# Optimization experiments

Hardware: AMD Instinct MI355X
Metric: run time of the kernel (lower is better)

The kernel has to match this reference:

```python
import jax, jax.numpy as jnp
import numpy as np

N = 50000       # nodes
E = 800000      # edges (before self-loops)
G = 512         # graphs in batch
IN_DIM = 128
OUT_DIM = 8
DIMS = [(IN_DIM, 32), (32, 64), (64, 128), (128, 64)]
EPS = 1e-5


def setup_inputs() -> dict:
    key = jax.random.key(0)
    ks = jax.random.split(key, 40)
    def nrm(k, shape, s=0.05):
        return jax.random.normal(k, shape, jnp.float32) * s
    inp = {}
    inp["x"] = jax.random.normal(ks[0], (N, IN_DIM), jnp.float32)
    inp["edge_index"] = jax.random.randint(ks[1], (2, E), 0, N, dtype=jnp.int32)
    inp["batch"] = jnp.sort(jax.random.randint(ks[2], (N,), 0, G, dtype=jnp.int32))
    for i, (din, dout) in enumerate(DIMS, 1):
        inp[f"W{i}"]  = nrm(ks[3 * i + 0], (din, dout))
        inp[f"as{i}"] = nrm(ks[3 * i + 1], (dout,))
        inp[f"ad{i}"] = nrm(ks[3 * i + 2], (dout,))
        inp[f"b{i}"]  = jnp.zeros((dout,), jnp.float32)
        inp[f"g{i}"]  = jnp.ones((dout,), jnp.float32)   # BN gamma
        inp[f"be{i}"] = jnp.zeros((dout,), jnp.float32)  # BN beta
    inp["Wf"] = nrm(ks[20], (64, 32)); inp["bf"] = jnp.zeros((32,), jnp.float32)
    inp["Wc"] = nrm(ks[21], (32, OUT_DIM)); inp["bc"] = jnp.zeros((OUT_DIM,), jnp.float32)
    return inp


def gat_conv(x, src, dst, W, a_s, a_d, b):
    """PyG GATConv, heads=1: linear (no bias) -> per-edge attention with
    leaky_relu(0.2) -> segment softmax over incoming edges -> scatter-add -> bias."""
    h = x @ W                                   # [N, F]
    a_src = h @ a_s                             # [N]
    a_dst = h @ a_d                             # [N]
    e = jax.nn.leaky_relu(a_src[src] + a_dst[dst], 0.2)   # [E+N]
    m = jax.ops.segment_max(e, dst, num_segments=N)
    w = jnp.exp(e - m[dst])
    denom = jax.ops.segment_sum(w, dst, num_segments=N)
    alpha = w / denom[dst]                      # self-loops guarantee denom > 0
    out = jax.ops.segment_sum(alpha[:, None] * h[src], dst, num_segments=N)
    return out + b


def batch_norm(x, g, be):
    mu = x.mean(axis=0)
    var = x.var(axis=0)                         # biased, as torch training BN
    return (x - mu) * jax.lax.rsqrt(var + EPS) * g + be


def reference(x, edge_index, batch,
              W1, as1, ad1, b1, g1, be1,
              W2, as2, ad2, b2, g2, be2,
              W3, as3, ad3, b3, g3, be3,
              W4, as4, ad4, b4, g4, be4,
              Wf, bf, Wc, bc):
    loops = jnp.arange(N, dtype=edge_index.dtype)
    src = jnp.concatenate([edge_index[0], loops])   # GATConv adds self-loops
    dst = jnp.concatenate([edge_index[1], loops])
    params = [(W1, as1, ad1, b1, g1, be1), (W2, as2, ad2, b2, g2, be2),
              (W3, as3, ad3, b3, g3, be3), (W4, as4, ad4, b4, g4, be4)]
    h = x
    for (W, a_s, a_d, b, g, be) in params:
        h = jax.nn.leaky_relu(gat_conv(h, src, dst, W, a_s, a_d, b), 0.01)
        h = batch_norm(h, g, be)
    pooled = jax.ops.segment_sum(h, batch, num_segments=G)   # global_add_pool
    z = jax.nn.leaky_relu(pooled @ Wf + bf, 0.01)
    return jax.nn.sigmoid(z @ Wc + bc)
```

## Files before the change

kernel.cpp:

```cpp
#include <hip/hip_runtime.h>
#include <math.h>

constexpr int BLK = 256;
constexpr int NBLKA = 256;
constexpr int NSH = 16;

static inline int cdiv(long a, long b) { return (int)((a + b - 1) / b); }

typedef __attribute__((ext_vector_type(8))) short short8;
typedef __attribute__((ext_vector_type(4))) float floatx4;

__device__ __forceinline__ unsigned short f2bf(float f) {
    unsigned u = __float_as_uint(f);
    unsigned r = u + 0x7fffu + ((u >> 16) & 1u);
    return (unsigned short)(r >> 16);
}
__device__ __forceinline__ float bf2f(unsigned short s) {
    return __uint_as_float(((unsigned)s) << 16);
}


__global__ void histA_k(const int* __restrict__ dst, int* __restrict__ histg,
                        int E, int nbkt, int chunk) {
    __shared__ int h[256];
    int tid = threadIdx.x, z = blockIdx.x;
    h[tid] = 0;
    __syncthreads();
    int e0 = z * chunk, e1 = min(E, e0 + chunk);
    for (int e = e0 + tid; e < e1; e += BLK) atomicAdd(&h[dst[e] >> 8], 1);
    __syncthreads();
    if (tid < nbkt) histg[z * nbkt + tid] = h[tid];
}

__global__ void blk_scan2_k(int* __restrict__ histg, int* __restrict__ bsum, int nbkt) {
    __shared__ int s[BLK];
    int t = threadIdx.x, b = blockIdx.x;
    int v = histg[t * nbkt + b];
    s[t] = v;
    __syncthreads();
    for (int o = 1; o < BLK; o <<= 1) {
        int tv = (t >= o) ? s[t - o] : 0;
        __syncthreads();
        s[t] += tv;
        __syncthreads();
    }
    histg[t * nbkt + b] = s[t] - v;
    if (t == BLK - 1) bsum[b] = s[t];
}

__global__ void scan_base_k(const int* __restrict__ bsum, int* __restrict__ bucket_base,
                            int nbkt, int E, int* __restrict__ gs, int* __restrict__ ge,
                            int G, float* __restrict__ bnstats) {
    __shared__ int s[BLK];
    int t = threadIdx.x;
    int v = (t < nbkt) ? bsum[t] : 0;
    s[t] = v;
    __syncthreads();
    for (int o = 1; o < BLK; o <<= 1) {
        int tv = (t >= o) ? s[t - o] : 0;
        __syncthreads();
        s[t] += tv;
        __syncthreads();
    }
    if (t < nbkt) bucket_base[t] = s[t] - v;
    if (t == 0) bucket_base[nbkt] = E;
    for (int i = t; i < G; i += BLK) { gs[i] = 0x7fffffff; ge[i] = -1; }
    for (int i = t; i < 4 * NSH * 256; i += BLK) bnstats[i] = 0.f;
}

__global__ void csrB_k(const unsigned* __restrict__ ebkt, const int* __restrict__ bucket_base,
                       int* __restrict__ off, unsigned short* __restrict__ csr,
                       const int* __restrict__ batch, int* __restrict__ gs,
                       int* __restrict__ ge, int N, int E, int nbkt) {
    __shared__ int dg[256];
    __shared__ int sc[256];
    int t = threadIdx.x, b = blockIdx.x;
    int n0 = b << 8;
    int cnt = min(256, N - n0);
    dg[t] = (t < cnt) ? 1 : 0;
    __syncthreads();
    int e0 = bucket_base[b], e1 = bucket_base[b + 1];
    for (int e = e0 + t; e < e1; e += BLK) atomicAdd(&dg[ebkt[e] >> 16], 1);
    __syncthreads();
    int d = dg[t];
    sc[t] = d;
    __syncthreads();
    for (int o = 1; o < BLK; o <<= 1) {
        int tv = (t >= o) ? sc[t - o] : 0;
        __syncthreads();
        sc[t] += tv;
        __syncthreads();
    }
    int loff = sc[t] - d;
    int csrbase = e0 + n0;
    if (t < cnt) {
        off[n0 + t] = csrbase + loff;
        csr[csrbase + loff] = (unsigned short)(n0 + t);
        dg[t] = loff + 1;
    }
    if (b == nbkt - 1 && t == 0) off[N] = E + N;
    int n = n0 + t;
    if (n < N) {
        int bb = batch[n];
        if (n == 0) gs[bb] = 0;
        else {
            int pb = batch[n - 1];
            if (pb != bb) { gs[bb] = n; ge[pb] = n - 1; }
        }
        if (n == N - 1) ge[bb] = N - 1;
    }
    __syncthreads();
    for (int e = e0 + t; e < e1; e += BLK) {
        unsigned w = ebkt[e];
        int pos = atomicAdd(&dg[w >> 16], 1);
        csr[csrbase + pos] = (unsigned short)(w & 0xffff);
    }
}

template <int K, int NOUT, bool AFP32, bool HASBN, bool DOTS, bool FIN>
__device__ __forceinline__ void gemm_body(int bx, const void* __restrict__ av,
                           const float* __restrict__ W,
                           const float* __restrict__ a_s, const float* __restrict__ a_d,
                           const float* __restrict__ bnst, const float* __restrict__ g_prev,
                           const float* __restrict__ be_prev, float invN,
                           const float* __restrict__ bias_l,
                           unsigned short* __restrict__ hb,
                           float* __restrict__ asrc, float* __restrict__ adst,
                           float* __restrict__ bn_out, int N) {
    constexpr int KF = K / 32;
    constexpr int NY = NOUT / 16;
    __shared__ float s_sca[K], s_scc[K];
    __shared__ float s_rs[DOTS ? K : 1], s_rd[DOTS ? K : 1], s_bd[2];
    __shared__ float sst[FIN ? 2 * NOUT : 1];
    int tid = threadIdx.x;
    if (FIN && tid < 2 * NOUT) sst[tid] = 0.f;
    if (tid < K) {
        float a = 1.f, c = 0.f;
        if (HASBN) {
            float su = 0.f, sq = 0.f;
#pragma unroll
            for (int s = 0; s < NSH; ++s) {
                su += bnst[s * 256 + tid];
                sq += bnst[s * 256 + 128 + tid];
            }
            float mu = su * invN;
            float var = sq * invN - mu * mu;
            a = g_prev[tid] * rsqrtf(var + 1e-5f);
            c = be_prev[tid] - mu * a;
        }
        s_sca[tid] = a; s_scc[tid] = c;
        if (DOTS) {
            const float* wr = W + (long)tid * NOUT;
            float rs = 0.f, rd = 0.f;
            for (int f = 0; f < NOUT; ++f) {
                float w = wr[f];
                rs += w * a_s[f];
                rd += w * a_d[f];
            }
            s_rs[tid] = rs; s_rd[tid] = rd;
        }
    }
    __syncthreads();
    if constexpr (DOTS) {
        if (tid < 2) {
            const float* r = tid ? s_rd : s_rs;
            float b = 0.f;
            for (int k = 0; k < K; ++k) b += s_scc[k] * r[k];
            s_bd[tid] = b;
        }
        __syncthreads();
    }

    int wave = tid >> 6;
    int lane = tid & 63;
    int quad = lane >> 4;
    int r16 = lane & 15;
    int blockbase = bx * 128;

    short8 afr[2][KF];
    bool valid[2];
#pragma unroll
    for (int rt = 0; rt < 2; ++rt) {
        int tilebase = blockbase + wave * 32 + rt * 16;
        valid[rt] = tilebase < N;
        if (!valid[rt]) continue;
        int arow = min(tilebase + r16, N - 1);
        if (AFP32) {
            const float* xr = (const float*)av + (long)arow * K;
#pragma unroll
            for (int kk = 0; kk < KF; ++kk) {
                float4 x0 = *(const float4*)(xr + kk * 32 + quad * 8);
                float4 x1 = *(const float4*)(xr + kk * 32 + quad * 8 + 4);
                short8 a;
                a[0] = (short)f2bf(x0.x); a[1] = (short)f2bf(x0.y);
                a[2] = (short)f2bf(x0.z); a[3] = (short)f2bf(x0.w);
                a[4] = (short)f2bf(x1.x); a[5] = (short)f2bf(x1.y);
                a[6] = (short)f2bf(x1.z); a[7] = (short)f2bf(x1.w);
                afr[rt][kk] = a;
            }
        } else {
            const unsigned short* hr = (const unsigned short*)av + (long)arow * K;
#pragma unroll
            for (int kk = 0; kk < KF; ++kk)
                afr[rt][kk] = *(const short8*)(hr + kk * 32 + quad * 8);
        }
        if constexpr (DOTS) {
            float ds = 0.f, dd = 0.f;
#pragma unroll
            for (int kk = 0; kk < KF; ++kk) {
                int kb = kk * 32 + quad * 8;
#pragma unroll
                for (int j = 0; j < 8; ++j) {
                    int k = kb + j;
                    float a = bf2f((unsigned short)afr[rt][kk][j]) * s_sca[k];
                    ds += a * s_rs[k];
                    dd += a * s_rd[k];
                }
            }
            ds += __shfl_xor(ds, 16, 64); ds += __shfl_xor(ds, 32, 64);
            dd += __shfl_xor(dd, 16, 64); dd += __shfl_xor(dd, 32, 64);
            int drow = tilebase + r16;
            if (quad == 0 && drow < N) {
                asrc[drow] = ds + s_bd[0];
                adst[drow] = dd + s_bd[1];
            }
        }
    }

#pragma unroll
    for (int y = 0; y < NY; ++y) {
        int col = y * 16 + r16;
        short8 bfr[KF];
        float biasp = 0.f;
#pragma unroll
        for (int kk = 0; kk < KF; ++kk) {
            short8 b;
#pragma unroll
            for (int j = 0; j < 8; ++j) {
                int k = kk * 32 + quad * 8 + j;
                float w = W[(long)k * NOUT + col];
                b[j] = (short)f2bf(s_sca[k] * w);
                biasp += s_scc[k] * w;
            }
            bfr[kk] = b;
        }
        biasp += __shfl_xor(biasp, 16, 64);
        biasp += __shfl_xor(biasp, 32, 64);
        if (FIN) biasp += bias_l[col];

        float sS = 0.f, sQ = 0.f;
#pragma unroll
        for (int rt = 0; rt < 2; ++rt) {
            if (!valid[rt]) continue;
            int tilebase = blockbase + wave * 32 + rt * 16;
            floatx4 acc = {0.f, 0.f, 0.f, 0.f};
#pragma unroll
            for (int kk = 0; kk < KF; ++kk)
                acc = __builtin_amdgcn_mfma_f32_16x16x32_bf16(afr[rt][kk], bfr[kk], acc, 0, 0, 0);
#pragma unroll
            for (int rr = 0; rr < 4; ++rr) {
                int srow = tilebase + quad * 4 + rr;
                if (srow < N) {
                    float v = acc[rr] + biasp;
                    if (FIN) {
                        v = v > 0.f ? v : 0.01f * v;
                        sS += v; sQ += v * v;
                    }
                    hb[(long)srow * NOUT + col] = f2bf(v);
                }
            }
        }
        if constexpr (FIN) {
            sS += __shfl_xor(sS, 16, 64); sS += __shfl_xor(sS, 32, 64);
            sQ += __shfl_xor(sQ, 16, 64); sQ += __shfl_xor(sQ, 32, 64);
            if (quad == 0) {
                atomicAdd(&sst[col], sS);
                atomicAdd(&sst[NOUT + col], sQ);
            }
        }
    }
    if constexpr (FIN) {
        __syncthreads();
        if (tid < 2 * NOUT) {
            float* base = bn_out + (bx & (NSH - 1)) * 256;
            int idx = (tid < NOUT) ? tid : (128 + tid - NOUT);
            atomicAdd(&base[idx], sst[tid]);
        }
    }
}

template <int K, int NOUT, bool AFP32, bool HASBN, bool DOTS, bool FIN>
__launch_bounds__(256)
__global__ void gemm_fused(const void* __restrict__ av, const float* __restrict__ W,
                           const float* __restrict__ a_s, const float* __restrict__ a_d,
                           const float* __restrict__ bnst, const float* __restrict__ g_prev,
                           const float* __restrict__ be_prev, float invN,
                           const float* __restrict__ bias_l,
                           unsigned short* __restrict__ hb,
                           float* __restrict__ asrc, float* __restrict__ adst,
                           float* __restrict__ bn_out, int N) {
    gemm_body<K, NOUT, AFP32, HASBN, DOTS, FIN>(blockIdx.x, av, W, a_s, a_d, bnst, g_prev,
                                                be_prev, invN, bias_l, hb, asrc, adst,
                                                bn_out, N);
}

__launch_bounds__(256)
__global__ void scatter_gemm0_k(const int* __restrict__ src, const int* __restrict__ dst,
                                const int* __restrict__ histg, const int* __restrict__ bucket_base,
                                unsigned* __restrict__ ebkt, int E, int nbkt, int chunk,
                                const float* __restrict__ x, const float* __restrict__ W0,
                                const float* __restrict__ as0, const float* __restrict__ ad0,
                                unsigned short* __restrict__ hb,
                                float* __restrict__ asrc, float* __restrict__ adst, int N) {
    if (blockIdx.x < NBLKA) {
        __shared__ int cur[256];
        int tid = threadIdx.x, z = blockIdx.x;
        if (tid < nbkt) cur[tid] = histg[z * nbkt + tid] + bucket_base[tid];
        __syncthreads();
        int e0 = z * chunk, e1 = min(E, e0 + chunk);
        for (int e = e0 + tid; e < e1; e += BLK) {
            int d = dst[e];
            int b = d >> 8;
            int pos = atomicAdd(&cur[b], 1);
            ebkt[pos] = ((unsigned)(d & 255) << 16) | (unsigned)src[e];
        }
    } else {
        gemm_body<128, 32, true, false, true, false>(blockIdx.x - NBLKA, x, W0, as0, ad0,
                                                     nullptr, nullptr, nullptr, 0.f, nullptr,
                                                     hb, asrc, adst, nullptr, N);
    }
}

template <int K, int NOUT>
__global__ void dots_k(const unsigned short* __restrict__ y, const float* __restrict__ W,
                       const float* __restrict__ a_s, const float* __restrict__ a_d,
                       const float* __restrict__ bnst, const float* __restrict__ g_prev,
                       const float* __restrict__ be_prev, float invN,
                       float* __restrict__ asrc, float* __restrict__ adst, int N) {
    __shared__ float crs[K], crd[K], s_scc[K], s_rs[K], s_rd[K], bd[2];
    int tid = threadIdx.x;
    if (tid < K) {
        float su = 0.f, sq = 0.f;
#pragma unroll
        for (int s = 0; s < NSH; ++s) {
            su += bnst[s * 256 + tid];
            sq += bnst[s * 256 + 128 + tid];
        }
        float mu = su * invN;
        float var = sq * invN - mu * mu;
        float a = g_prev[tid] * rsqrtf(var + 1e-5f);
        float c = be_prev[tid] - mu * a;
        const float* wr = W + (long)tid * NOUT;
        float rs = 0.f, rd = 0.f;
        for (int f = 0; f < NOUT; ++f) {
            float w = wr[f];
            rs += w * a_s[f];
            rd += w * a_d[f];
        }
        crs[tid] = a * rs; crd[tid] = a * rd;
        s_scc[tid] = c; s_rs[tid] = rs; s_rd[tid] = rd;
    }
    __syncthreads();
    if (tid < 2) {
        const float* r = tid ? s_rd : s_rs;
        float b = 0.f;
        for (int k = 0; k < K; ++k) b += s_scc[k] * r[k];
        bd[tid] = b;
    }
    __syncthreads();
    int n = blockIdx.x * blockDim.x + tid;
    if (n >= N) return;
    const unsigned short* yr = y + (long)n * K;
    float ds = bd[0], dd = bd[1];
#pragma unroll
    for (int kk = 0; kk < K / 8; ++kk) {
        short8 v8 = *(const short8*)(yr + kk * 8);
#pragma unroll
        for (int j = 0; j < 8; ++j) {
            float yv = bf2f((unsigned short)v8[j]);
            ds += yv * crs[kk * 8 + j];
            dd += yv * crd[kk * 8 + j];
        }
    }
    asrc[n] = ds;
    adst[n] = dd;
}

template <int K, int NOUT>
__launch_bounds__(256)
__global__ void gather_gemm_k(const int* __restrict__ off,
                              const unsigned short* __restrict__ csr,
                              const float* __restrict__ asrc, const float* __restrict__ adst,
                              const unsigned short* __restrict__ y,
                              const float* __restrict__ W,
                              const float* __restrict__ bnst, const float* __restrict__ g_prev,
                              const float* __restrict__ be_prev, float invN,
                              const float* __restrict__ bias_l,
                              unsigned short* __restrict__ out_h,
                              float* __restrict__ bn_out, int N) {
    constexpr int FPL = K / 4;
    constexpr int NV = FPL / 8;
    constexpr int KF = K / 32;
    constexpr int NY = NOUT / 16;
    constexpr int LROW = K + 8;
    __shared__ __align__(16) unsigned short agg[64][LROW];
    __shared__ float s_sca[K], s_scc[K];
    __shared__ float sst[2 * NOUT];
    int tid = threadIdx.x;
    if (tid < 2 * NOUT) sst[tid] = 0.f;
    if (tid < K) {
        float su = 0.f, sq = 0.f;
#pragma unroll
        for (int s = 0; s < NSH; ++s) {
            su += bnst[s * 256 + tid];
            sq += bnst[s * 256 + 128 + tid];
        }
        float mu = su * invN;
        float var = sq * invN - mu * mu;
        float a = g_prev[tid] * rsqrtf(var + 1e-5f);
        s_sca[tid] = a;
        s_scc[tid] = be_prev[tid] - mu * a;
    }

    int lrow = tid >> 2;
    int l = tid & 3;
    int d = blockIdx.x * 64 + lrow;
    bool active = d < N;
    int p0 = 0, p1 = 0;
    float ad = 0.f;
    if (active) { p0 = off[d]; p1 = off[d + 1]; ad = adst[d]; }
    const int f0 = l * FPL;

    float acc[FPL];
#pragma unroll
    for (int i = 0; i < FPL; ++i) acc[i] = 0.f;
    float sum = 0.f;

#pragma unroll 2
    for (int p = p0; p < p1; ++p) {
        int s = csr[p];
        float e = asrc[s] + ad;
        e = e > 0.f ? e : 0.2f * e;
        float w = __expf(e);
        sum += w;
        const unsigned short* hr = y + (long)s * K + f0;
#pragma unroll
        for (int v = 0; v < NV; ++v) {
            const uint4 hv = *(const uint4*)(hr + v * 8);
            acc[v * 8 + 0] += w * bf2f((unsigned short)(hv.x & 0xffff));
            acc[v * 8 + 1] += w * bf2f((unsigned short)(hv.x >> 16));
            acc[v * 8 + 2] += w * bf2f((unsigned short)(hv.y & 0xffff));
            acc[v * 8 + 3] += w * bf2f((unsigned short)(hv.y >> 16));
            acc[v * 8 + 4] += w * bf2f((unsigned short)(hv.z & 0xffff));
            acc[v * 8 + 5] += w * bf2f((unsigned short)(hv.z >> 16));
            acc[v * 8 + 6] += w * bf2f((unsigned short)(hv.w & 0xffff));
            acc[v * 8 + 7] += w * bf2f((unsigned short)(hv.w >> 16));
        }
    }
    float inv = active ? (1.f / sum) : 0.f;

#pragma unroll
    for (int v = 0; v < NV; ++v) {
        unsigned pk[4];
#pragma unroll
        for (int i = 0; i < 4; ++i) {
            float v0 = active ? acc[v * 8 + 2 * i] * inv : 0.f;
            float v1 = active ? acc[v * 8 + 2 * i + 1] * inv : 0.f;
            pk[i] = (unsigned)f2bf(v0) | ((unsigned)f2bf(v1) << 16);
        }
        *(uint4*)&agg[lrow][f0 + v * 8] = uint4{pk[0], pk[1], pk[2], pk[3]};
    }
    __syncthreads();

    int wave = tid >> 6;
    int lane = tid & 63;
    int quad = lane >> 4;
    int r16 = lane & 15;
    int tilebase = blockIdx.x * 64 + wave * 16;
    int lrow2 = wave * 16 + r16;

    short8 afr[KF];
#pragma unroll
    for (int kk = 0; kk < KF; ++kk)
        afr[kk] = *(const short8*)&agg[lrow2][kk * 32 + quad * 8];

#pragma unroll
    for (int yy = 0; yy < NY; ++yy) {
        int col = yy * 16 + r16;
        short8 bfr[KF];
        float biasp = 0.f;
#pragma unroll
        for (int kk = 0; kk < KF; ++kk) {
            short8 b;
#pragma unroll
            for (int j = 0; j < 8; ++j) {
                int k = kk * 32 + quad * 8 + j;
                float w = W[(long)k * NOUT + col];
                b[j] = (short)f2bf(s_sca[k] * w);
                biasp += s_scc[k] * w;
            }
            bfr[kk] = b;
        }
        biasp += __shfl_xor(biasp, 16, 64);
        biasp += __shfl_xor(biasp, 32, 64);
        biasp += bias_l[col];

        floatx4 acc4 = {0.f, 0.f, 0.f, 0.f};
#pragma unroll
        for (int kk = 0; kk < KF; ++kk)
            acc4 = __builtin_amdgcn_mfma_f32_16x16x32_bf16(afr[kk], bfr[kk], acc4, 0, 0, 0);

        float sS = 0.f, sQ = 0.f;
#pragma unroll
        for (int rr = 0; rr < 4; ++rr) {
            int srow = tilebase + quad * 4 + rr;
            if (srow < N) {
                float v = acc4[rr] + biasp;
                v = v > 0.f ? v : 0.01f * v;
                sS += v; sQ += v * v;
                out_h[(long)srow * NOUT + col] = f2bf(v);
            }
        }
        sS += __shfl_xor(sS, 16, 64); sS += __shfl_xor(sS, 32, 64);
        sQ += __shfl_xor(sQ, 16, 64); sQ += __shfl_xor(sQ, 32, 64);
        if (quad == 0) {
            atomicAdd(&sst[col], sS);
            atomicAdd(&sst[NOUT + col], sQ);
        }
    }
    __syncthreads();
    if (tid < 2 * NOUT) {
        float* base = bn_out + (blockIdx.x & (NSH - 1)) * 256;
        int idx = (tid < NOUT) ? tid : (128 + tid - NOUT);
        atomicAdd(&base[idx], sst[tid]);
    }
}

template <int DOUT, int FPL>
__global__ void gather_fused(const int* __restrict__ off,
                             const unsigned short* __restrict__ csr,
                             const float* __restrict__ asrc, const float* __restrict__ adst,
                             const unsigned short* __restrict__ hb,
                             const float* __restrict__ b,
                             unsigned short* __restrict__ out,
                             float* __restrict__ bn, int N) {
    constexpr int TPN = DOUT / FPL;
    constexpr int NV = FPL / 8;
    __shared__ float sst[2 * DOUT];
    int tid = threadIdx.x;
    if (tid < 2 * DOUT) sst[tid] = 0.f;
    __syncthreads();

    int t = blockIdx.x * blockDim.x + tid;
    int d = t / TPN;
    int l = t % TPN;
    bool active = d < N;
    int lane = tid & 63;

    int p0 = 0, p1 = 0;
    float ad = 0.f;
    if (active) { p0 = off[d]; p1 = off[d + 1]; ad = adst[d]; }
    const int f0 = l * FPL;

    float acc[FPL];
#pragma unroll
    for (int i = 0; i < FPL; ++i) acc[i] = 0.f;
    float sum = 0.f;

#pragma unroll 2
    for (int p = p0; p < p1; ++p) {
        int s = csr[p];
        float e = asrc[s] + ad;
        e = e > 0.f ? e : 0.2f * e;
        float w = __expf(e);
        sum += w;
        const unsigned short* hr = hb + (long)s * DOUT + f0;
#pragma unroll
        for (int v = 0; v < NV; ++v) {
            const uint4 hv = *(const uint4*)(hr + v * 8);
            acc[v * 8 + 0] += w * bf2f((unsigned short)(hv.x & 0xffff));
            acc[v * 8 + 1] += w * bf2f((unsigned short)(hv.x >> 16));
            acc[v * 8 + 2] += w * bf2f((unsigned short)(hv.y & 0xffff));
            acc[v * 8 + 3] += w * bf2f((unsigned short)(hv.y >> 16));
            acc[v * 8 + 4] += w * bf2f((unsigned short)(hv.z & 0xffff));
            acc[v * 8 + 5] += w * bf2f((unsigned short)(hv.z >> 16));
            acc[v * 8 + 6] += w * bf2f((unsigned short)(hv.w & 0xffff));
            acc[v * 8 + 7] += w * bf2f((unsigned short)(hv.w >> 16));
        }
    }
    float inv = active ? (1.f / sum) : 0.f;

#pragma unroll
    for (int v = 0; v < NV; ++v) {
        float4 b0 = *(const float4*)(b + f0 + v * 8);
        float4 b1 = *(const float4*)(b + f0 + v * 8 + 4);
        float bbv[8] = {b0.x, b0.y, b0.z, b0.w, b1.x, b1.y, b1.z, b1.w};
        unsigned pk[4];
#pragma unroll
        for (int i = 0; i < 4; ++i) {
            float v0 = acc[v * 8 + 2 * i] * inv + bbv[2 * i];
            float v1 = acc[v * 8 + 2 * i + 1] * inv + bbv[2 * i + 1];
            v0 = v0 > 0.f ? v0 : 0.01f * v0;
            v1 = v1 > 0.f ? v1 : 0.01f * v1;
            if (!active) { v0 = 0.f; v1 = 0.f; }
            acc[v * 8 + 2 * i] = v0;
            acc[v * 8 + 2 * i + 1] = v1;
            pk[i] = (unsigned)f2bf(v0) | ((unsigned)f2bf(v1) << 16);
        }
        if (active)
            *(uint4*)(out + (long)d * DOUT + f0 + v * 8) = uint4{pk[0], pk[1], pk[2], pk[3]};
    }

#pragma unroll
    for (int i = 0; i < FPL; ++i) {
        float s = acc[i];
        float q = s * s;
#pragma unroll
        for (int o = TPN; o < 64; o <<= 1) {
            s += __shfl_xor(s, o, 64);
            q += __shfl_xor(q, o, 64);
        }
        if (lane < TPN) {
            atomicAdd(&sst[f0 + i], s);
            atomicAdd(&sst[DOUT + f0 + i], q);
        }
    }
    __syncthreads();
    if (tid < 2 * DOUT) {
        float* base = bn + (blockIdx.x & (NSH - 1)) * 256;
        int idx = (tid < DOUT) ? tid : (128 + tid - DOUT);
        atomicAdd(&base[idx], sst[tid]);
    }
}

__global__ void pool_head_k(const unsigned short* __restrict__ h, const int* __restrict__ gs,
                            const int* __restrict__ ge, const float* __restrict__ bnst,
                            const float* __restrict__ g4, const float* __restrict__ be4,
                            float invN, const float* __restrict__ Wf,
                            const float* __restrict__ bf, const float* __restrict__ Wc,
                            const float* __restrict__ bc, float* __restrict__ out) {
    int g = blockIdx.x;
    int t = threadIdx.x;
    int f = t & 63, sub = t >> 6;
    __shared__ float pp[4][64];
    __shared__ float p[64];
    __shared__ float z[32];
    int s0 = gs[g], s1 = ge[g];
    float acc = 0.f;
    if (s0 <= s1)
        for (int n = s0 + sub; n <= s1; n += 4) acc += bf2f(h[(long)n * 64 + f]);
    pp[sub][f] = acc;
    __syncthreads();
    if (t < 64) {
        float su = 0.f, sq = 0.f;
#pragma unroll
        for (int s = 0; s < NSH; ++s) {
            su += bnst[s * 256 + t];
            sq += bnst[s * 256 + 128 + t];
        }
        float mu = su * invN;
        float var = sq * invN - mu * mu;
        float a = g4[t] * rsqrtf(var + 1e-5f);
        float c = be4[t] - mu * a;
        float cnt = (s0 <= s1) ? (float)(s1 - s0 + 1) : 0.f;
        p[t] = a * (pp[0][t] + pp[1][t] + pp[2][t] + pp[3][t]) + cnt * c;
    }
    __syncthreads();
    if (t < 32) {
        float zacc = bf[t];
#pragma unroll
        for (int ff = 0; ff < 64; ++ff) zacc += p[ff] * Wf[ff * 32 + t];
        z[t] = zacc > 0.f ? zacc : 0.01f * zacc;
    }
    __syncthreads();
    if (t < 8) {
        float oacc = bc[t];
#pragma unroll
        for (int o = 0; o < 32; ++o) oacc += z[o] * Wc[o * 8 + t];
        out[(long)g * 8 + t] = 1.f / (1.f + __expf(-oacc));
    }
}

extern "C" void kernel_launch(void* const* d_in, const int* in_sizes, int n_in,
                              void* d_out, int out_size, void* d_ws, size_t ws_size,
                              hipStream_t stream) {
    const float* x   = (const float*)d_in[0];
    const int* ei    = (const int*)d_in[1];
    const int* batch = (const int*)d_in[2];
    const int N  = in_sizes[2];
    const int E  = in_sizes[1] / 2;
    const int ET = E + N;
    const int G  = out_size / 8;
    const int* src = ei;
    const int* dst = ei + E;

    const float *W[4], *as_[4], *ad_[4], *bb[4], *gg[4], *be_[4];
    for (int i = 0; i < 4; ++i) {
        W[i]   = (const float*)d_in[3 + 6 * i];
        as_[i] = (const float*)d_in[4 + 6 * i];
        ad_[i] = (const float*)d_in[5 + 6 * i];
        bb[i]  = (const float*)d_in[6 + 6 * i];
        gg[i]  = (const float*)d_in[7 + 6 * i];
        be_[i] = (const float*)d_in[8 + 6 * i];
    }
    const float* Wf = (const float*)d_in[27];
    const float* bfp = (const float*)d_in[28];
    const float* Wc = (const float*)d_in[29];
    const float* bc = (const float*)d_in[30];

    float* ws = (float*)d_ws;
    long off_ = 0;
    auto alloc = [&](long nelem) { float* p = ws + off_; off_ += (nelem + 3) & ~3L; return p; };
    unsigned short* h2a = (unsigned short*)alloc((long)N * 64);
    unsigned short* h2b = (unsigned short*)alloc((long)N * 64);
    unsigned short* hb  = (unsigned short*)alloc((long)N * 64);
    float* asrc     = alloc(N);
    float* adst     = alloc(N);
    float* bnstats  = alloc((long)4 * NSH * 256);
    unsigned* ebkt  = (unsigned*)alloc(E);
    int* histg      = (int*)alloc((long)NBLKA * 256);
    int* bucket_base = (int*)alloc(260);
    int* bsum       = (int*)alloc(256);
    int* off        = (int*)alloc(N + 1);
    unsigned short* csr = (unsigned short*)alloc(ET / 2 + 2);
    int* gs         = (int*)alloc(G);
    int* ge         = (int*)alloc(G);
    (void)ws_size; (void)n_in;

    const int nbkt = cdiv(N, 256);
    const int chunk = cdiv(E, NBLKA);
    const float invN = 1.f / (float)N;
    float* bn0 = bnstats + 0L * NSH * 256;
    float* bn1 = bnstats + 1L * NSH * 256;
    float* bn2 = bnstats + 2L * NSH * 256;
    float* bn3 = bnstats + 3L * NSH * 256;

    histA_k<<<NBLKA, BLK, 0, stream>>>(dst, histg, E, nbkt, chunk);
    blk_scan2_k<<<nbkt, BLK, 0, stream>>>(histg, bsum, nbkt);
    scan_base_k<<<1, BLK, 0, stream>>>(bsum, bucket_base, nbkt, E, gs, ge, G, bnstats);
    scatter_gemm0_k<<<NBLKA + cdiv(N, 128), BLK, 0, stream>>>(
        src, dst, histg, bucket_base, ebkt, E, nbkt, chunk,
        x, W[0], as_[0], ad_[0], hb, asrc, adst, N);
    csrB_k<<<nbkt, BLK, 0, stream>>>(ebkt, bucket_base, off, csr, batch, gs, ge, N, E, nbkt);

    gather_fused<32, 8><<<cdiv((long)N * 4, BLK), BLK, 0, stream>>>(
        off, csr, asrc, adst, hb, bb[0], h2b, bn0, N);

    dots_k<32, 64><<<cdiv(N, BLK), BLK, 0, stream>>>(
        h2b, W[1], as_[1], ad_[1], bn0, gg[0], be_[0], invN, asrc, adst, N);
    gather_gemm_k<32, 64><<<cdiv(N, 64), BLK, 0, stream>>>(
        off, csr, asrc, adst, h2b, W[1], bn0, gg[0], be_[0], invN, bb[1],
        h2a, bn1, N);

    dots_k<64, 128><<<cdiv(N, BLK), BLK, 0, stream>>>(
        h2a, W[2], as_[2], ad_[2], bn1, gg[1], be_[1], invN, asrc, adst, N);
    gather_gemm_k<64, 128><<<cdiv(N, 64), BLK, 0, stream>>>(
        off, csr, asrc, adst, h2a, W[2], bn1, gg[1], be_[1], invN, bb[2],
        h2b, bn2, N);

    gemm_fused<128, 64, false, true, true, false><<<cdiv(N, 128), 256, 0, stream>>>(
        h2b, W[3], as_[3], ad_[3], bn2, gg[2], be_[2], invN, nullptr, hb,
        asrc, adst, nullptr, N);
    gather_fused<64, 16><<<cdiv((long)N * 4, BLK), BLK, 0, stream>>>(
        off, csr, asrc, adst, hb, bb[3], h2a, bn3, N);

    pool_head_k<<<G, 256, 0, stream>>>(h2a, gs, ge, bn3, gg[3], be_[3],
                                       invN, Wf, bfp, Wc, bc, (float*)d_out);
}
```

Before: 302.8 us.

## Sort destination nodes by in-degree to balance gather work across waves

Builds a degree histogram during CSR construction, scans it, and produces a permutation of nodes sorted by in-degree (a counting sort). All gather kernels then process nodes in permuted order, so lanes within a wave have similar edge-loop trip counts and spend less time idle on divergent loop lengths. Outputs are written back to each node's original row. The cost is two extra small kernels, an indirection load per node, and scattered output writes that lose the locality of processing consecutive node ids.

Measured after the change: 309.4 us. 2.2% more time.

```diff
diff --git a/kernel.cpp b/kernel.cpp
--- a/kernel.cpp
+++ b/kernel.cpp
@@ -50,7 +50,7 @@
 
 __global__ void scan_base_k(const int* __restrict__ bsum, int* __restrict__ bucket_base,
                             int nbkt, int E, int* __restrict__ gs, int* __restrict__ ge,
-                            int G, float* __restrict__ bnstats) {
+                            int G, float* __restrict__ bnstats, int* __restrict__ deghist) {
     __shared__ int s[BLK];
     int t = threadIdx.x;
     int v = (t < nbkt) ? bsum[t] : 0;
@@ -64,6 +64,7 @@
     }
     if (t < nbkt) bucket_base[t] = s[t] - v;
     if (t == 0) bucket_base[nbkt] = E;
+    deghist[t] = 0;
     for (int i = t; i < G; i += BLK) { gs[i] = 0x7fffffff; ge[i] = -1; }
     for (int i = t; i < 4 * NSH * 256; i += BLK) bnstats[i] = 0.f;
 }
@@ -71,18 +72,22 @@
 __global__ void csrB_k(const unsigned* __restrict__ ebkt, const int* __restrict__ bucket_base,
                        int* __restrict__ off, unsigned short* __restrict__ csr,
                        const int* __restrict__ batch, int* __restrict__ gs,
-                       int* __restrict__ ge, int N, int E, int nbkt) {
+                       int* __restrict__ ge, int* __restrict__ deghist,
+                       int N, int E, int nbkt) {
     __shared__ int dg[256];
     __shared__ int sc[256];
+    __shared__ int dh[256];
     int t = threadIdx.x, b = blockIdx.x;
     int n0 = b << 8;
     int cnt = min(256, N - n0);
     dg[t] = (t < cnt) ? 1 : 0;
+    dh[t] = 0;
     __syncthreads();
     int e0 = bucket_base[b], e1 = bucket_base[b + 1];
     for (int e = e0 + t; e < e1; e += BLK) atomicAdd(&dg[ebkt[e] >> 16], 1);
     __syncthreads();
     int d = dg[t];
+    if (t < cnt) atomicAdd(&dh[min(d, 255)], 1);
     sc[t] = d;
     __syncthreads();
     for (int o = 1; o < BLK; o <<= 1) {
@@ -114,6 +119,43 @@
         unsigned w = ebkt[e];
         int pos = atomicAdd(&dg[w >> 16], 1);
         csr[csrbase + pos] = (unsigned short)(w & 0xffff);
+    }
+    if (dh[t]) atomicAdd(&deghist[t], dh[t]);
+}
+
+__global__ void deg_scan_k(const int* __restrict__ deghist, int* __restrict__ degcursor) {
+    __shared__ int s[256];
+    int t = threadIdx.x;
+    int v = deghist[t];
+    s[t] = v;
+    __syncthreads();
+    for (int o = 1; o < 256; o <<= 1) {
+        int tv = (t >= o) ? s[t - o] : 0;
+        __syncthreads();
+        s[t] += tv;
+        __syncthreads();
+    }
+    degcursor[t] = s[t] - v;
+}
+
+__global__ void perm_k(const int* __restrict__ off, int* __restrict__ degcursor,
+                       int* __restrict__ perm, int N) {
+    __shared__ int hist[256], base[256], cur[256];
+    int t = threadIdx.x;
+    hist[t] = 0; cur[t] = 0;
+    __syncthreads();
+    int n = blockIdx.x * 256 + t;
+    int dgr = 0;
+    if (n < N) {
+        dgr = min(off[n + 1] - off[n], 255);
+        atomicAdd(&hist[dgr], 1);
+    }
+    __syncthreads();
+    if (hist[t] > 0) base[t] = atomicAdd(&degcursor[t], hist[t]);
+    __syncthreads();
+    if (n < N) {
+        int r = atomicAdd(&cur[dgr], 1);
+        perm[base[dgr] + r] = n;
     }
 }
 
@@ -396,6 +438,7 @@
                               const float* __restrict__ bnst, const float* __restrict__ g_prev,
                               const float* __restrict__ be_prev, float invN,
                               const float* __restrict__ bias_l,
+                              const int* __restrict__ perm,
                               unsigned short* __restrict__ out_h,
                               float* __restrict__ bn_out, int N) {
     constexpr int FPL = K / 4;
@@ -404,6 +447,7 @@
     constexpr int NY = NOUT / 16;
     constexpr int LROW = K + 8;
     __shared__ __align__(16) unsigned short agg[64][LROW];
+    __shared__ int s_nid[64];
     __shared__ float s_sca[K], s_scc[K];
     __shared__ float sst[2 * NOUT];
     int tid = threadIdx.x;
@@ -424,8 +468,10 @@
 
     int lrow = tid >> 2;
     int l = tid & 3;
-    int d = blockIdx.x * 64 + lrow;
-    bool active = d < N;
+    int nd = blockIdx.x * 64 + lrow;
+    bool active = nd < N;
+    int d = active ? perm[nd] : -1;
+    if (l == 0) s_nid[lrow] = d;
     int p0 = 0, p1 = 0;
     float ad = 0.f;
     if (active) { p0 = off[d]; p1 = off[d + 1]; ad = adst[d]; }
@@ -476,7 +522,6 @@
     int lane = tid & 63;
     int quad = lane >> 4;
     int r16 = lane & 15;
-    int tilebase = blockIdx.x * 64 + wave * 16;
     int lrow2 = wave * 16 + r16;
 
     short8 afr[KF];
@@ -513,12 +558,12 @@
         float sS = 0.f, sQ = 0.f;
 #pragma unroll
         for (int rr = 0; rr < 4; ++rr) {
-            int srow = tilebase + quad * 4 + rr;
-            if (srow < N) {
+            int node = s_nid[wave * 16 + quad * 4 + rr];
+            if (node >= 0) {
                 float v = acc4[rr] + biasp;
                 v = v > 0.f ? v : 0.01f * v;
                 sS += v; sQ += v * v;
-                out_h[(long)srow * NOUT + col] = f2bf(v);
+                out_h[(long)node * NOUT + col] = f2bf(v);
             }
         }
         sS += __shfl_xor(sS, 16, 64); sS += __shfl_xor(sS, 32, 64);
@@ -542,6 +587,7 @@
                              const float* __restrict__ asrc, const float* __restrict__ adst,
                              const unsigned short* __restrict__ hb,
                              const float* __restrict__ b,
+                             const int* __restrict__ perm,
                              unsigned short* __restrict__ out,
                              float* __restrict__ bn, int N) {
     constexpr int TPN = DOUT / FPL;
@@ -552,9 +598,10 @@
     __syncthreads();
 
     int t = blockIdx.x * blockDim.x + tid;
-    int d = t / TPN;
+    int nd = t / TPN;
     int l = t % TPN;
-    bool active = d < N;
+    bool active = nd < N;
+    int d = active ? perm[nd] : 0;
     int lane = tid & 63;
 
     int p0 = 0, p1 = 0;
@@ -725,6 +772,9 @@
     unsigned short* csr = (unsigned short*)alloc(ET / 2 + 2);
     int* gs         = (int*)alloc(G);
     int* ge         = (int*)alloc(G);
+    int* deghist    = (int*)alloc(256);
+    int* degcursor  = (int*)alloc(256);
+    int* perm       = (int*)alloc(N);
     (void)ws_size; (void)n_in;
 
     const int nbkt = cdiv(N, 256);
@@ -737,32 +787,35 @@
 
     histA_k<<<NBLKA, BLK, 0, stream>>>(dst, histg, E, nbkt, chunk);
     blk_scan2_k<<<nbkt, BLK, 0, stream>>>(histg, bsum, nbkt);
-    scan_base_k<<<1, BLK, 0, stream>>>(bsum, bucket_base, nbkt, E, gs, ge, G, bnstats);
+    scan_base_k<<<1, BLK, 0, stream>>>(bsum, bucket_base, nbkt, E, gs, ge, G, bnstats, deghist);
     scatter_gemm0_k<<<NBLKA + cdiv(N, 128), BLK, 0, stream>>>(
         src, dst, histg, bucket_base, ebkt, E, nbkt, chunk,
         x, W[0], as_[0], ad_[0], hb, asrc, adst, N);
-    csrB_k<<<nbkt, BLK, 0, stream>>>(ebkt, bucket_base, off, csr, batch, gs, ge, N, E, nbkt);
+    csrB_k<<<nbkt, BLK, 0, stream>>>(ebkt, bucket_base, off, csr, batch, gs, ge, deghist,
+                                     N, E, nbkt);
+    deg_scan_k<<<1, 256, 0, stream>>>(deghist, degcursor);
+    perm_k<<<nbkt, 256, 0, stream>>>(off, degcursor, perm, N);
 
     gather_fused<32, 8><<<cdiv((long)N * 4, BLK), BLK, 0, stream>>>(
-        off, csr, asrc, adst, hb, bb[0], h2b, bn0, N);
+        off, csr, asrc, adst, hb, bb[0], perm, h2b, bn0, N);
 
     dots_k<32, 64><<<cdiv(N, BLK), BLK, 0, stream>>>(
         h2b, W[1], as_[1], ad_[1], bn0, gg[0], be_[0], invN, asrc, adst, N);
     gather_gemm_k<32, 64><<<cdiv(N, 64), BLK, 0, stream>>>(
-        off, csr, asrc, adst, h2b, W[1], bn0, gg[0], be_[0], invN, bb[1],
+        off, csr, asrc, adst, h2b, W[1], bn0, gg[0], be_[0], invN, bb[1], perm,
         h2a, bn1, N);
 
     dots_k<64, 128><<<cdiv(N, BLK), BLK, 0, stream>>>(
         h2a, W[2], as_[2], ad_[2], bn1, gg[1], be_[1], invN, asrc, adst, N);
     gather_gemm_k<64, 128><<<cdiv(N, 64), BLK, 0, stream>>>(
-        off, csr, asrc, adst, h2a, W[2], bn1, gg[1], be_[1], invN, bb[2],
+        off, csr, asrc, adst, h2a, W[2], bn1, gg[1], be_[1], invN, bb[2], perm,
         h2b, bn2, N);
 
     gemm_fused<128, 64, false, true, true, false><<<cdiv(N, 128), 256, 0, stream>>>(
         h2b, W[3], as_[3], ad_[3], bn2, gg[2], be_[2], invN, nullptr, hb,
         asrc, adst, nullptr, N);
     gather_fused<64, 16><<<cdiv((long)N * 4, BLK), BLK, 0, stream>>>(
-        off, csr, asrc, adst, hb, bb[3], h2a, bn3, N);
+        off, csr, asrc, adst, hb, bb[3], perm, h2a, bn3, N);
 
     pool_head_k<<<G, 256, 0, stream>>>(h2a, gs, ge, bn3, gg[3], be_[3],
                                        invN, Wf, bfp, Wc, bc, (float*)d_out);
```
